# Kernel tuning notes

Measured on AMD Instinct MI355X. Metric: run time of the kernel, lower is better.

## Reference

```python
import jax, jax.numpy as jnp
import numpy as np

N_NODES = 100000
N_EDGES = 1600000
IN_CH, HID_CH, OUT_CH = 128, 128, 64


def _sage_conv(x, src, dst, deg_inv, W_l, b_l, W_r):
    # PyG SAGEConv (mean aggr): out = lin_l(mean_{j in N(i)} x_j) + lin_r(x_i)
    msg = x[src]                                   # [E, C_in] gather
    agg = jax.ops.segment_sum(msg, dst, num_segments=N_NODES)  # [N, C_in]
    agg = agg * deg_inv[:, None]
    return agg @ W_l.T + b_l + x @ W_r.T


def setup_inputs() -> dict:
    key = jax.random.key(0)
    ks = jax.random.split(key, 10)
    x = jax.random.normal(ks[0], (N_NODES, IN_CH), dtype=jnp.float32)
    edge_attr = jax.random.normal(ks[1], (N_EDGES, 4), dtype=jnp.float32)
    edge_index = jax.random.randint(ks[2], (2, N_EDGES), 0, N_NODES, dtype=jnp.int32)
    dims = [(IN_CH, HID_CH), (HID_CH, HID_CH), (HID_CH, OUT_CH)]
    params = {}
    for i, (cin, cout) in enumerate(dims):
        s = 1.0 / np.sqrt(cin)
        params[f"W_l{i}"] = jax.random.uniform(ks[3 + 2 * i], (cout, cin), minval=-s, maxval=s, dtype=jnp.float32)
        params[f"b_l{i}"] = jnp.zeros((cout,), dtype=jnp.float32)
        params[f"W_r{i}"] = jax.random.uniform(ks[4 + 2 * i], (cout, cin), minval=-s, maxval=s, dtype=jnp.float32)
    return {"x": x, "edge_attr": edge_attr, "edge_index": edge_index, **params}


def reference(x, edge_attr, edge_index,
              W_l0, b_l0, W_r0,
              W_l1, b_l1, W_r1,
              W_l2, b_l2, W_r2):
    src, dst = edge_index[0], edge_index[1]
    deg = jax.ops.segment_sum(jnp.ones((N_EDGES,), jnp.float32), dst, num_segments=N_NODES)
    deg_inv = 1.0 / jnp.maximum(deg, 1.0)
    layers = [(W_l0, b_l0, W_r0), (W_l1, b_l1, W_r1), (W_l2, b_l2, W_r2)]
    h = x
    for i, (Wl, bl, Wr) in enumerate(layers):
        h = _sage_conv(h, src, dst, deg_inv, Wl, bl, Wr)
        if i != len(layers) - 1:
            h = jax.nn.relu(h)
            # dropout is identity in eval mode (training=False)
    return h
```

## Files before the change

kernel.cpp:

```cpp
#include <hip/hip_runtime.h>
#include <cstdint>

#define N_NODES 100000
#define N_EDGES 1600000

constexpr int NCB = 196;
constexpr int HB  = 391;

typedef __attribute__((ext_vector_type(8))) short short8;
typedef __attribute__((ext_vector_type(4))) float f32x4;

__device__ inline uint32_t fbits(float f) { union { float f; uint32_t u; } c; c.f = f; return c.u; }
__device__ inline float bfloat(uint32_t u) { union { uint32_t u; float f; } c; c.u = u; return c.f; }

__device__ inline void bsplit(float a, short& hi, short& lo) {
    uint32_t h = fbits(a) & 0xFFFF0000u;
    float fl = a - bfloat(h);
    hi = (short)(h >> 16);
    lo = (short)(fbits(fl) >> 16);
}

__device__ inline ushort f2bf(float f) {
    uint32_t u = fbits(f);
    return (ushort)((u + 0x7FFFu + ((u >> 16) & 1u)) >> 16);
}


__global__ __launch_bounds__(256)
void hist_kernel(const int* __restrict__ dst, int* __restrict__ H) {
    __shared__ int h[NCB];
    for (int i = threadIdx.x; i < NCB; i += 256) h[i] = 0;
    __syncthreads();
    int e0 = blockIdx.x * 4096;
    #pragma unroll
    for (int it = 0; it < 16; ++it) {
        int e = e0 + it * 256 + threadIdx.x;
        if (e < N_EDGES) atomicAdd(&h[dst[e] >> 9], 1);
    }
    __syncthreads();
    for (int i = threadIdx.x; i < NCB; i += 256) H[blockIdx.x * NCB + i] = h[i];
}

__global__ __launch_bounds__(256)
void scanbase_kernel(int* __restrict__ H, int* __restrict__ boff) {
    __shared__ int tot[NCB];
    __shared__ int base[NCB + 1];
    int j = threadIdx.x;
    if (j < NCB) {
        int s = 0;
        for (int b = 0; b < HB; ++b) s += H[b * NCB + j];
        tot[j] = s;
    }
    __syncthreads();
    if (j == 0) {
        int run = 0;
        for (int k = 0; k < NCB; ++k) { base[k] = run; run += tot[k]; }
        base[NCB] = run;
    }
    __syncthreads();
    if (j <= NCB) boff[j] = base[j];
    if (j < NCB) {
        int run = base[j];
        for (int b = 0; b < HB; ++b) {
            int v = H[b * NCB + j];
            H[b * NCB + j] = run;
            run += v;
        }
    }
}

__global__ __launch_bounds__(256)
void scatter_kernel(const int* __restrict__ src, const int* __restrict__ dst,
                    const int* __restrict__ H, uint32_t* __restrict__ ebuf) {
    __shared__ int cur[NCB];
    for (int i = threadIdx.x; i < NCB; i += 256) cur[i] = H[blockIdx.x * NCB + i];
    __syncthreads();
    int e0 = blockIdx.x * 4096;
    #pragma unroll
    for (int it = 0; it < 16; ++it) {
        int e = e0 + it * 256 + threadIdx.x;
        if (e < N_EDGES) {
            int d = dst[e];
            int p = atomicAdd(&cur[d >> 9], 1);
            ebuf[p] = ((uint32_t)src[e] << 9) | (uint32_t)(d & 511);
        }
    }
}


__global__ __launch_bounds__(256)
void bucket_csr(const uint32_t* __restrict__ ebuf, const int* __restrict__ boff,
                int* __restrict__ off, float* __restrict__ dinv,
                int* __restrict__ ssrc) {
    __shared__ int deg[512];
    __shared__ int cur[512];
    __shared__ int wsum[4];
    int t = threadIdx.x, lane = t & 63, w = t >> 6;
    int j = blockIdx.x;
    int base = boff[j], end = boff[j + 1];
    int node0 = j << 9;

    deg[t] = 0; deg[t + 256] = 0;
    __syncthreads();

    for (int p = base + t; p < end; p += 256)
        atomicAdd(&deg[ebuf[p] & 511u], 1);
    __syncthreads();

    int d0 = deg[2 * t], d1 = deg[2 * t + 1];
    int s = d0 + d1;
    int incl = s;
    #pragma unroll
    for (int d = 1; d < 64; d <<= 1) {
        int u = __shfl_up(incl, d);
        if (lane >= d) incl += u;
    }
    if (lane == 63) wsum[w] = incl;
    __syncthreads();
    if (t < 4) {
        int v = wsum[t];
        int iv = v;
        #pragma unroll
        for (int d = 1; d < 4; d <<= 1) {
            int u = __shfl_up(iv, d, 4);
            if (t >= d) iv += u;
        }
        wsum[t] = iv - v;
    }
    __syncthreads();
    int ebase = wsum[w] + (incl - s);
    cur[2 * t] = ebase;
    cur[2 * t + 1] = ebase + d0;
    int n0 = node0 + 2 * t, n1 = n0 + 1;
    if (n0 < N_NODES) {
        off[n0] = base + ebase;
        dinv[n0] = 1.0f / (float)max(d0, 1);
    }
    if (n1 < N_NODES) {
        off[n1] = base + ebase + d0;
        dinv[n1] = 1.0f / (float)max(d1, 1);
    }
    if (j == 0 && t == 0) off[N_NODES] = N_EDGES;
    __syncthreads();

    for (int p = base + t; p < end; p += 256) {
        uint32_t ent = ebuf[p];
        int pos = atomicAdd(&cur[ent & 511u], 1);
        ssrc[base + pos] = (int)(ent >> 9);
    }
}


__global__ void wfrag_kernel(const float* __restrict__ W1, const float* __restrict__ W2,
                             int C1, int NCT, int ntask,
                             short* __restrict__ fhi, short* __restrict__ flo) {
    int tau = blockIdx.x * 256 + threadIdx.x;
    if (tau >= ntask) return;
    int lane = tau & 63;
    int ct = (tau >> 6) % NCT;
    int ks = (tau >> 6) / NCT;
    int col = ct * 16 + (lane & 15);
    int k = ks * 32 + (lane >> 4) * 8;
    const float* p = (col < C1) ? &W1[(size_t)col * 128 + k]
                                : &W2[(size_t)(col - C1) * 128 + k];
    short8 h8, l8;
    #pragma unroll
    for (int j = 0; j < 8; ++j) {
        short h, l;
        bsplit(p[j], h, l);
        h8[j] = h; l8[j] = l;
    }
    *reinterpret_cast<short8*>(&fhi[(size_t)tau * 8]) = h8;
    *reinterpret_cast<short8*>(&flo[(size_t)tau * 8]) = l8;
}


template<int C1, int C2>
__global__ __launch_bounds__(256)
void gemm_mfma(const float* __restrict__ H, const short* __restrict__ Wfhi,
               const short* __restrict__ Wflo, const float* __restrict__ bias2,
               ushort* __restrict__ out1, float* __restrict__ out2) {
    constexpr int COUT = C1 + C2;
    constexpr int CT = COUT / 64;
    constexpr int NCT = COUT / 16;
    __shared__ short Ahi[64 * 128];
    __shared__ short Alo[64 * 128];
    int t = threadIdx.x;
    int l = t & 63, w = t >> 6;
    int lr = l & 15, kg = l >> 4;
    int r0 = blockIdx.x * 64;
    int c_base = w * (COUT / 4);
    const bool is1 = (c_base < C1);

    #pragma unroll
    for (int it = 0; it < 4; ++it) {
        int lin = t + it * 256;
        int row = lin >> 4, ch = lin & 15;
        float av[8];
        if (r0 + row < N_NODES) {
            const float* p = &H[(size_t)(r0 + row) * 128 + ch * 8];
            float4 v0 = *reinterpret_cast<const float4*>(p);
            float4 v1 = *reinterpret_cast<const float4*>(p + 4);
            av[0] = v0.x; av[1] = v0.y; av[2] = v0.z; av[3] = v0.w;
            av[4] = v1.x; av[5] = v1.y; av[6] = v1.z; av[7] = v1.w;
        } else {
            #pragma unroll
            for (int j = 0; j < 8; ++j) av[j] = 0.f;
        }
        short8 h8, l8;
        #pragma unroll
        for (int j = 0; j < 8; ++j) {
            short h, lo2;
            bsplit(av[j], h, lo2);
            h8[j] = h; l8[j] = lo2;
        }
        int off = row * 128 + ((ch ^ (row & 7)) << 3);
        *reinterpret_cast<short8*>(&Ahi[off]) = h8;
        *reinterpret_cast<short8*>(&Alo[off]) = l8;
    }
    __syncthreads();

    f32x4 acc[4][CT];
    #pragma unroll
    for (int m = 0; m < 4; ++m)
        #pragma unroll
        for (int c = 0; c < CT; ++c)
            acc[m][c] = (f32x4){0.f, 0.f, 0.f, 0.f};

    #pragma unroll
    for (int ks = 0; ks < 4; ++ks) {
        int ch = ks * 4 + kg;
        short8 ahi[4], alo[4];
        #pragma unroll
        for (int m = 0; m < 4; ++m) {
            int row = m * 16 + lr;
            int off = row * 128 + ((ch ^ (row & 7)) << 3);
            ahi[m] = *reinterpret_cast<const short8*>(&Ahi[off]);
            alo[m] = *reinterpret_cast<const short8*>(&Alo[off]);
        }
        short8 bhi[CT], blo[CT];
        #pragma unroll
        for (int c = 0; c < CT; ++c) {
            int ctg = w * CT + c;
            size_t fo = ((size_t)(ks * NCT + ctg) * 64 + l) * 8;
            bhi[c] = *reinterpret_cast<const short8*>(&Wfhi[fo]);
            blo[c] = *reinterpret_cast<const short8*>(&Wflo[fo]);
        }
        #pragma unroll
        for (int m = 0; m < 4; ++m)
            #pragma unroll
            for (int c = 0; c < CT; ++c) {
                acc[m][c] = __builtin_amdgcn_mfma_f32_16x16x32_bf16(ahi[m], bhi[c], acc[m][c], 0, 0, 0);
                acc[m][c] = __builtin_amdgcn_mfma_f32_16x16x32_bf16(ahi[m], blo[c], acc[m][c], 0, 0, 0);
                acc[m][c] = __builtin_amdgcn_mfma_f32_16x16x32_bf16(alo[m], bhi[c], acc[m][c], 0, 0, 0);
            }
    }

    if (is1) {
        #pragma unroll
        for (int c = 0; c < CT; ++c) {
            int col = c_base + c * 16 + lr;
            #pragma unroll
            for (int m = 0; m < 4; ++m)
                #pragma unroll
                for (int r = 0; r < 4; ++r) {
                    int row = r0 + m * 16 + kg * 4 + r;
                    if (row < N_NODES)
                        out1[(size_t)row * C1 + col] = f2bf(acc[m][c][r]);
                }
        }
    } else {
        #pragma unroll
        for (int c = 0; c < CT; ++c) {
            int col = c_base - C1 + c * 16 + lr;
            float bb = bias2[col];
            #pragma unroll
            for (int m = 0; m < 4; ++m)
                #pragma unroll
                for (int r = 0; r < 4; ++r) {
                    int row = r0 + m * 16 + kg * 4 + r;
                    if (row < N_NODES)
                        out2[(size_t)row * C2 + col] = acc[m][c][r] + bb;
                }
        }
    }
}


template<int C, bool RELU>
__global__ __launch_bounds__(256)
void agg_kernel(const ushort* __restrict__ Y, const int* __restrict__ off,
                const int* __restrict__ ssrc, const float* __restrict__ dinv,
                float* out) {
    constexpr int CQ = C / 8;
    int tid = blockIdx.x * 256 + threadIdx.x;
    int i = tid / CQ, cq = tid % CQ;
    if (i >= N_NODES) return;
    int p0 = off[i], p1 = off[i + 1];
    float acc[8] = {0.f, 0.f, 0.f, 0.f, 0.f, 0.f, 0.f, 0.f};
    for (int p = p0; p < p1; ++p) {
        int s = ssrc[p];
        uint4 v = *reinterpret_cast<const uint4*>(&Y[(size_t)s * C + cq * 8]);
        uint32_t wd[4] = {v.x, v.y, v.z, v.w};
        #pragma unroll
        for (int j = 0; j < 4; ++j) {
            acc[2 * j]     += bfloat(wd[j] << 16);
            acc[2 * j + 1] += bfloat(wd[j] & 0xFFFF0000u);
        }
    }
    float di = dinv[i];
    float* op = &out[(size_t)i * C + cq * 8];
    float4 z0 = *reinterpret_cast<const float4*>(op);
    float4 z1 = *reinterpret_cast<const float4*>(op + 4);
    float zz[8] = {z0.x, z0.y, z0.z, z0.w, z1.x, z1.y, z1.z, z1.w};
    float r[8];
    #pragma unroll
    for (int j = 0; j < 8; ++j) {
        r[j] = acc[j] * di + zz[j];
        if (RELU) r[j] = fmaxf(r[j], 0.f);
    }
    *reinterpret_cast<float4*>(op)     = make_float4(r[0], r[1], r[2], r[3]);
    *reinterpret_cast<float4*>(op + 4) = make_float4(r[4], r[5], r[6], r[7]);
}


extern "C" void kernel_launch(void* const* d_in, const int* in_sizes, int n_in,
                              void* d_out, int out_size, void* d_ws, size_t ws_size,
                              hipStream_t stream) {
    const float* x   = (const float*)d_in[0];
    const int*   ei  = (const int*)d_in[2];
    const float* Wl0 = (const float*)d_in[3];
    const float* bl0 = (const float*)d_in[4];
    const float* Wr0 = (const float*)d_in[5];
    const float* Wl1 = (const float*)d_in[6];
    const float* bl1 = (const float*)d_in[7];
    const float* Wr1 = (const float*)d_in[8];
    const float* Wl2 = (const float*)d_in[9];
    const float* bl2 = (const float*)d_in[10];
    const float* Wr2 = (const float*)d_in[11];
    float* out = (float*)d_out;

    char* ws = (char*)d_ws;
    int*      H    = (int*)(ws + 0);
    int*      boff = (int*)(ws + (size_t)(384 << 10));
    int*      off  = (int*)(ws + (size_t)(512 << 10));
    float*    dinv = (float*)(ws + (size_t)(960 << 10));
    uint32_t* ebuf = (uint32_t*)(ws + (size_t)(1400 << 10));
    int*      ssrc = (int*)(ws + (size_t)(1400 << 10) + (size_t)(7 << 20));
    short* w0hi = (short*)(ws + (size_t)(16 << 20));
    short* w0lo = w0hi + 32768;
    short* w1hi = w0lo + 32768;
    short* w1lo = w1hi + 32768;
    short* w2hi = w1lo + 32768;
    short* w2lo = w2hi + 16384;
    ushort* Ybf = (ushort*)(ws + (size_t)(18 << 20));
    float* bufB = (float*)(ws + (size_t)(46 << 20));

    const int* srcp = ei;
    const int* dstp = ei + N_EDGES;

    hist_kernel<<<HB, 256, 0, stream>>>(dstp, H);
    scanbase_kernel<<<1, 256, 0, stream>>>(H, boff);
    scatter_kernel<<<HB, 256, 0, stream>>>(srcp, dstp, H, ebuf);
    bucket_csr<<<NCB, 256, 0, stream>>>(ebuf, boff, off, dinv, ssrc);

    wfrag_kernel<<<16, 256, 0, stream>>>(Wl0, Wr0, 128, 16, 4096, w0hi, w0lo);
    wfrag_kernel<<<16, 256, 0, stream>>>(Wl1, Wr1, 128, 16, 4096, w1hi, w1lo);
    wfrag_kernel<<<8, 256, 0, stream>>>(Wl2, Wr2, 64, 8, 2048, w2hi, w2lo);

    int ggrid = (N_NODES + 63) / 64;
    int agrid128 = (N_NODES * 16 + 255) / 256;
    int agrid64  = (N_NODES * 8 + 255) / 256;

    gemm_mfma<128, 128><<<ggrid, 256, 0, stream>>>(x, w0hi, w0lo, bl0, Ybf, bufB);
    agg_kernel<128, true><<<agrid128, 256, 0, stream>>>(Ybf, off, ssrc, dinv, bufB);

    gemm_mfma<128, 128><<<ggrid, 256, 0, stream>>>(bufB, w1hi, w1lo, bl1, Ybf, bufB);
    agg_kernel<128, true><<<agrid128, 256, 0, stream>>>(Ybf, off, ssrc, dinv, bufB);

    gemm_mfma<64, 64><<<ggrid, 256, 0, stream>>>(bufB, w2hi, w2lo, bl2, Ybf, out);
    agg_kernel<64, false><<<agrid64, 256, 0, stream>>>(Ybf, off, ssrc, dinv, out);
}
```

Before: 393.9 us.

## Assign one wavefront per node in aggregation with edge-parallel lanes and shuffle reduction

The aggregation kernel previously gave each node 16 (or 8) lanes, each walking that node's edges one at a time. Now each 64-lane wavefront handles one node: lanes are split into edge slots that process different edges at once, two per iteration, and a butterfly shuffle reduction then combines the partial sums. This is meant to raise memory-level parallelism and shorten the per-thread serial gather chain for average degree 16. In exchange it adds shuffle work, and lanes sit idle for low-degree nodes.

New measurement: 390.5 us. No clear change (-0.9%).

```diff
diff --git a/kernel.cpp b/kernel.cpp
--- a/kernel.cpp
+++ b/kernel.cpp
@@ -289,38 +289,55 @@
 
 template<int C, bool RELU>
 __global__ __launch_bounds__(256)
-void agg_kernel(const ushort* __restrict__ Y, const int* __restrict__ off,
-                const int* __restrict__ ssrc, const float* __restrict__ dinv,
-                float* out) {
-    constexpr int CQ = C / 8;
-    int tid = blockIdx.x * 256 + threadIdx.x;
-    int i = tid / CQ, cq = tid % CQ;
-    if (i >= N_NODES) return;
+void agg_wave(const ushort* __restrict__ Y, const int* __restrict__ off,
+              const int* __restrict__ ssrc, const float* __restrict__ dinv,
+              float* __restrict__ out) {
+    constexpr int NCH = C / 8;
+    constexpr int ESL = 64 / NCH;
+    int t = threadIdx.x, l = t & 63;
+    int i = blockIdx.x * 4 + (t >> 6);
+    int chunk = l & (NCH - 1);
+    int eslot = l / NCH;
     int p0 = off[i], p1 = off[i + 1];
+
     float acc[8] = {0.f, 0.f, 0.f, 0.f, 0.f, 0.f, 0.f, 0.f};
-    for (int p = p0; p < p1; ++p) {
-        int s = ssrc[p];
-        uint4 v = *reinterpret_cast<const uint4*>(&Y[(size_t)s * C + cq * 8]);
-        uint32_t wd[4] = {v.x, v.y, v.z, v.w};
-        #pragma unroll
-        for (int j = 0; j < 4; ++j) {
-            acc[2 * j]     += bfloat(wd[j] << 16);
-            acc[2 * j + 1] += bfloat(wd[j] & 0xFFFF0000u);
-        }
-    }
-    float di = dinv[i];
-    float* op = &out[(size_t)i * C + cq * 8];
-    float4 z0 = *reinterpret_cast<const float4*>(op);
-    float4 z1 = *reinterpret_cast<const float4*>(op + 4);
-    float zz[8] = {z0.x, z0.y, z0.z, z0.w, z1.x, z1.y, z1.z, z1.w};
-    float r[8];
-    #pragma unroll
-    for (int j = 0; j < 8; ++j) {
-        r[j] = acc[j] * di + zz[j];
-        if (RELU) r[j] = fmaxf(r[j], 0.f);
-    }
-    *reinterpret_cast<float4*>(op)     = make_float4(r[0], r[1], r[2], r[3]);
-    *reinterpret_cast<float4*>(op + 4) = make_float4(r[4], r[5], r[6], r[7]);
+    for (int p = p0; p < p1; p += 2 * ESL) {
+        #pragma unroll
+        for (int u = 0; u < 2; ++u) {
+            int q = p + u * ESL + eslot;
+            if (q < p1) {
+                int s = ssrc[q];
+                uint4 v = *reinterpret_cast<const uint4*>(&Y[(size_t)s * C + chunk * 8]);
+                uint32_t wd[4] = {v.x, v.y, v.z, v.w};
+                #pragma unroll
+                for (int j = 0; j < 4; ++j) {
+                    acc[2 * j]     += bfloat(wd[j] << 16);
+                    acc[2 * j + 1] += bfloat(wd[j] & 0xFFFF0000u);
+                }
+            }
+        }
+    }
+    #pragma unroll
+    for (int d = NCH; d < 64; d <<= 1)
+        #pragma unroll
+        for (int j = 0; j < 8; ++j)
+            acc[j] += __shfl_xor(acc[j], d);
+
+    if (eslot == 0) {
+        float di = dinv[i];
+        float* op = &out[(size_t)i * C + chunk * 8];
+        float4 z0 = *reinterpret_cast<const float4*>(op);
+        float4 z1 = *reinterpret_cast<const float4*>(op + 4);
+        float zz[8] = {z0.x, z0.y, z0.z, z0.w, z1.x, z1.y, z1.z, z1.w};
+        float r[8];
+        #pragma unroll
+        for (int j = 0; j < 8; ++j) {
+            r[j] = acc[j] * di + zz[j];
+            if (RELU) r[j] = fmaxf(r[j], 0.f);
+        }
+        *reinterpret_cast<float4*>(op)     = make_float4(r[0], r[1], r[2], r[3]);
+        *reinterpret_cast<float4*>(op + 4) = make_float4(r[4], r[5], r[6], r[7]);
+    }
 }
 
 
@@ -369,15 +386,14 @@
     wfrag_kernel<<<8, 256, 0, stream>>>(Wl2, Wr2, 64, 8, 2048, w2hi, w2lo);
 
     int ggrid = (N_NODES + 63) / 64;
-    int agrid128 = (N_NODES * 16 + 255) / 256;
-    int agrid64  = (N_NODES * 8 + 255) / 256;
+    int wgrid = (N_NODES + 3) / 4;
 
     gemm_mfma<128, 128><<<ggrid, 256, 0, stream>>>(x, w0hi, w0lo, bl0, Ybf, bufB);
-    agg_kernel<128, true><<<agrid128, 256, 0, stream>>>(Ybf, off, ssrc, dinv, bufB);
+    agg_wave<128, true><<<wgrid, 256, 0, stream>>>(Ybf, off, ssrc, dinv, bufB);
 
     gemm_mfma<128, 128><<<ggrid, 256, 0, stream>>>(bufB, w1hi, w1lo, bl1, Ybf, bufB);
-    agg_kernel<128, true><<<agrid128, 256, 0, stream>>>(Ybf, off, ssrc, dinv, bufB);
+    agg_wave<128, true><<<wgrid, 256, 0, stream>>>(Ybf, off, ssrc, dinv, bufB);
 
     gemm_mfma<64, 64><<<ggrid, 256, 0, stream>>>(bufB, w2hi, w2lo, bl2, Ybf, out);
-    agg_kernel<64, false><<<agrid64, 256, 0, stream>>>(Ybf, off, ssrc, dinv, out);
-}
+    agg_wave<64, false><<<wgrid, 256, 0, stream>>>(Ybf, off, ssrc, dinv, out);
+}
```
